# Kernel tuning notes

Measured on AMD Instinct MI355X. Metric: run time of the kernel, lower is better.

The kernel has to match this reference:

```python
import jax, jax.numpy as jnp
import numpy as np

B, D, E = 128, 1024, 1024   # batch, word_rnn_size, word_encoding_size
NV, NL = 36, 20             # visual regions, language memory slots
T = 4                       # max_att_step
EPS = 0.01                  # opt.epsilon
SCALE = 0.02


def _lstm_cell(x, h, c, Wih, Whh, bih, bhh):
    # torch.nn.LSTMCell gate order: i, f, g, o
    g = x @ Wih.T + bih + h @ Whh.T + bhh
    i, f, gg, o = jnp.split(g, 4, axis=-1)
    c2 = jax.nn.sigmoid(f) * c + jax.nn.sigmoid(i) * jnp.tanh(gg)
    h2 = jax.nn.sigmoid(o) * jnp.tanh(c2)
    return h2, c2


def _kv_attention(h_att, vkey, vval, lkey, lval, kvs):
    # stand-in for the externally-passed kv_attention module:
    # scaled dot-product attention over visual and language memories
    q = h_att + kvs                                   # [B,D]
    inv = 1.0 / np.sqrt(D)
    va = jax.nn.softmax(jnp.einsum('bnd,bd->bn', vkey, q) * inv, axis=-1)
    vctx = jnp.einsum('bn,bnd->bd', va, vval)
    la = jax.nn.softmax(jnp.einsum('bmd,bd->bm', lkey, q) * inv, axis=-1)
    lctx = jnp.einsum('bm,bmd->bd', la, lval)
    return vctx, lctx, jnp.tanh(kvs + vctx + lctx)


def _update_kv(out, vkey, lkey):
    # stand-in for the externally-passed update_kv module
    return vkey + 0.01 * out[:, None, :], lkey + 0.01 * out[:, None, :]


def _forward(xt, fc_feats, visual_value, visual_key, lang_value, lang_key,
             kv_state, state_h, state_c,
             att_Wih, att_Whh, att_bih, att_bhh,
             lang_Wih, lang_Whh, lang_bih, lang_bhh,
             conf_W1, conf_b1, conf_W2, conf_b2,
             it, max_att_step):
    word_exist = (it > 0).astype(jnp.float32)         # [B]
    prev_h = state_h[-1]
    # att_lstm input is constant across halting steps (state is not updated in the loop)
    att_in = jnp.concatenate([prev_h, fc_feats, xt], axis=1)  # [B, E+2D]
    z1 = jnp.zeros((B, 1), jnp.float32)
    zD = jnp.zeros((B, D), jnp.float32)
    zB = jnp.zeros((B,), jnp.float32)
    carry0 = (z1, jnp.ones((B, 1), jnp.float32), zD, zD, zD, zD, zD, zB,
              visual_key, lang_key, kv_state)

    def body(carry, i):
        accum, sel, hA, cA, hL, cL, outA, cost, vkey, lkey, kvs = carry
        h_att, c_att = _lstm_cell(att_in, state_h[0], state_c[0],
                                  att_Wih, att_Whh, att_bih, att_bhh)
        vctx, lctx, kvs = _kv_attention(h_att, vkey, visual_value, lkey, lang_value, kvs)
        lang_in = jnp.concatenate([vctx, lctx, h_att], axis=1)  # [B,3D]
        h_lang, c_lang = _lstm_cell(lang_in, state_h[1], state_c[1],
                                    lang_Wih, lang_Whh, lang_bih, lang_bhh)
        out = h_lang  # F.dropout in eval mode is identity
        vkey, lkey = _update_kv(out, vkey, lkey)
        # confidence MLP: Linear -> ReLU -> Linear -> Sigmoid
        p = jax.nn.sigmoid(jax.nn.relu(h_lang @ conf_W1.T + conf_b1) @ conf_W2.T + conf_b2)  # [B,1]
        beta = p * (1.0 - accum)
        accum = accum + beta * sel
        hA = hA + beta * h_att * sel
        cA = cA + beta * c_att * sel
        hL = hL + beta * h_lang * sel
        cL = cL + beta * c_lang * sel
        outA = outA + beta * out * sel
        cost = cost + (i + 1.0) * (1.0 - p[:, 0]) * sel[:, 0]
        sel = jax.lax.stop_gradient((accum < 1.0 - EPS).astype(jnp.float32)) * sel
        return (accum, sel, hA, cA, hL, cL, outA, cost, vkey, lkey, kvs), None

    carry, _ = jax.lax.scan(body, carry0, jnp.arange(max_att_step, dtype=jnp.float32))
    accum, sel, hA, cA, hL, cL, outA, cost, vkey, lkey, kvs = carry
    hA = hA / accum
    cA = cA / accum
    hL = hL / accum
    cL = cL / accum
    outA = outA / accum
    new_h = jnp.stack([hA, hL])
    new_c = jnp.stack([cA, cL])
    return outA, vkey, lkey, cost * word_exist, new_h, new_c, kvs


def setup_inputs() -> dict:
    ks = jax.random.split(jax.random.key(0), 20)
    n = lambda k, s, sc=1.0: jax.random.normal(k, s, dtype=jnp.float32) * sc
    return {
        'xt': n(ks[0], (B, E)),
        'it': jax.random.randint(ks[1], (B,), 0, 9487, dtype=jnp.int32),
        'fc_feats': n(ks[2], (B, D)),
        'visual_value': n(ks[3], (B, NV, D)),
        'visual_key': n(ks[4], (B, NV, D)),
        'lang_value': n(ks[5], (B, NL, D)),
        'lang_key': n(ks[6], (B, NL, D)),
        'kv_state': n(ks[7], (B, D)),
        'state_h': n(ks[8], (2, B, D)),
        'state_c': n(ks[9], (2, B, D)),
        'max_att_step': T,
        'att_Wih': n(ks[10], (4 * D, E + 2 * D), SCALE),
        'att_Whh': n(ks[11], (4 * D, D), SCALE),
        'att_bih': jnp.zeros((4 * D,), jnp.float32),
        'att_bhh': jnp.zeros((4 * D,), jnp.float32),
        'lang_Wih': n(ks[12], (4 * D, 3 * D), SCALE),
        'lang_Whh': n(ks[13], (4 * D, D), SCALE),
        'lang_bih': jnp.zeros((4 * D,), jnp.float32),
        'lang_bhh': jnp.zeros((4 * D,), jnp.float32),
        'conf_W1': n(ks[14], (D, D), SCALE),
        'conf_b1': jnp.zeros((D,), jnp.float32),
        'conf_W2': n(ks[15], (1, D), SCALE),
        'conf_b2': jnp.zeros((1,), jnp.float32),
    }


def reference(xt, it, fc_feats, visual_value, visual_key, lang_value, lang_key,
              kv_state, state_h, state_c, max_att_step,
              att_Wih, att_Whh, att_bih, att_bhh,
              lang_Wih, lang_Whh, lang_bih, lang_bhh,
              conf_W1, conf_b1, conf_W2, conf_b2):
    return _forward(xt, fc_feats, visual_value, visual_key, lang_value, lang_key,
                    kv_state, state_h, state_c,
                    att_Wih, att_Whh, att_bih, att_bhh,
                    lang_Wih, lang_Whh, lang_bih, lang_bhh,
                    conf_W1, conf_b1, conf_W2, conf_b2,
                    it, max_att_step)
```

## Files before the change

kernel.cpp:

```cpp
#include <hip/hip_runtime.h>
#include <hip/hip_bf16.h>

constexpr int B  = 128;
constexpr int D  = 1024;
constexpr int NV = 36;
constexpr int NL = 20;
constexpr int BD = B * D;
constexpr float EPS = 0.01f;
constexpr int NSLOT = 8;

constexpr long SL  = 524288;
constexpr long SLB = 2097152;
constexpr long OFF_GPA   = 0;
constexpr long OFF_GPLB  = OFF_GPA + 8 * SL;
constexpr long OFF_LBASE = OFF_GPLB + 8 * SL;
constexpr long OFF_GPB   = OFF_LBASE + SL;
constexpr long OFF_GPC0  = OFF_GPB + 2 * SLB;
constexpr long OFF_GPC1  = OFF_GPC0 + 524288;
constexpr long OFF_HATT2 = OFF_GPC1 + 524288;
constexpr long OFF_CATT2 = OFF_HATT2 + BD;
constexpr long OFF_HLB   = OFF_CATT2 + BD;
constexpr long OFF_CLB   = OFF_HLB + 524288;
constexpr long OFF_VCTXB = OFF_CLB + 524288;
constexpr long OFF_LCTXB = OFF_VCTXB + 524288;
constexpr long OFF_S2    = OFF_LCTXB + 524288;
constexpr long OFF_VVB   = OFF_S2 + BD;
constexpr long OFF_LVB   = OFF_VVB + 2359296;

typedef float f32x4 __attribute__((ext_vector_type(4)));
typedef short s16x8 __attribute__((ext_vector_type(8)));

__device__ __forceinline__ float sigf(float x) { return 1.f / (1.f + expf(-x)); }

__device__ __forceinline__ short f2bf(float f) {
  __hip_bfloat16 h = __float2bfloat16(f);
  return *reinterpret_cast<short*>(&h);
}
__device__ __forceinline__ float bf2f(short s) {
  unsigned u = ((unsigned)(unsigned short)s) << 16;
  return __uint_as_float(u);
}

__device__ __forceinline__ f32x4 LD4(const float* p) { return *(const f32x4*)p; }
__device__ __forceinline__ void ST4(float* p, f32x4 v) { *(f32x4*)p = v; }

struct GemmArgs {
  const float* A[NSLOT];
  const float* W[NSLOT];
  long wstride[NSLOT];
  int klen;
};

__global__ __launch_bounds__(256, 2) void gemm_mfma(GemmArgs ga, int N,
                                                    long pstride,
                                                    float* __restrict__ gpart) {
  const int z = blockIdx.z;
  const float* __restrict__ A = ga.A[z];
  const float* __restrict__ W = ga.W[z];
  const long wstr = ga.wstride[z];
  const int brow = blockIdx.y * 128;
  const int bcol = blockIdx.x * 64;
  float* __restrict__ out = gpart + (long)z * pstride;

  __shared__ __align__(16) short As[2][128][72];
  __shared__ __align__(16) short Bs[2][64][72];

  const int tid = threadIdx.x;
  const int wave = tid >> 6, lane = tid & 63;
  const int wr = wave >> 1, wc = wave & 1;
  const int lrow = lane & 15;
  const int lk8  = (lane >> 4) * 8;
  const int sr = tid >> 4;
  const int sc4 = (tid & 15) * 4;

  f32x4 acc[4][2];
#pragma unroll
  for (int m = 0; m < 4; ++m)
#pragma unroll
    for (int n = 0; n < 2; ++n) acc[m][n] = (f32x4){0.f, 0.f, 0.f, 0.f};

  float4 ra[8], rw[4];
#define LOAD_TILE(KT)                                                          \
  {                                                                            \
    const int kb = (KT) * 64;                                                  \
    _Pragma("unroll") for (int i = 0; i < 8; ++i) {                            \
      const int r = sr + i * 16;                                               \
      ra[i] = *(const float4*)(A + (long)(brow + r) * 1024 + kb + sc4);        \
    }                                                                          \
    _Pragma("unroll") for (int i = 0; i < 4; ++i) {                            \
      const int r = sr + i * 16;                                               \
      rw[i] = *(const float4*)(W + (long)(bcol + r) * wstr + kb + sc4);        \
    }                                                                          \
  }
#define WRITE_TILE(BUF)                                                        \
  {                                                                            \
    _Pragma("unroll") for (int i = 0; i < 8; ++i) {                            \
      const int r = sr + i * 16;                                               \
      *(short4*)(&As[BUF][r][sc4]) =                                           \
          short4{f2bf(ra[i].x), f2bf(ra[i].y), f2bf(ra[i].z), f2bf(ra[i].w)};  \
    }                                                                          \
    _Pragma("unroll") for (int i = 0; i < 4; ++i) {                            \
      const int r = sr + i * 16;                                               \
      *(short4*)(&Bs[BUF][r][sc4]) =                                           \
          short4{f2bf(rw[i].x), f2bf(rw[i].y), f2bf(rw[i].z), f2bf(rw[i].w)};  \
    }                                                                          \
  }

  const int ntiles = ga.klen / 64;
  LOAD_TILE(0);
  WRITE_TILE(0);
  __syncthreads();
  for (int kt = 0; kt < ntiles; ++kt) {
    const int cur = kt & 1;
    const bool more = (kt + 1 < ntiles);
    if (more) LOAD_TILE(kt + 1);
#pragma unroll
    for (int kk = 0; kk < 64; kk += 32) {
      s16x8 af[4], bf[2];
#pragma unroll
      for (int m = 0; m < 4; ++m)
        af[m] = *(const s16x8*)(&As[cur][wr * 64 + m * 16 + lrow][kk + lk8]);
#pragma unroll
      for (int n = 0; n < 2; ++n)
        bf[n] = *(const s16x8*)(&Bs[cur][wc * 32 + n * 16 + lrow][kk + lk8]);
#pragma unroll
      for (int m = 0; m < 4; ++m)
#pragma unroll
        for (int n = 0; n < 2; ++n)
          acc[m][n] = __builtin_amdgcn_mfma_f32_16x16x32_bf16(
              af[m], bf[n], acc[m][n], 0, 0, 0);
    }
    if (more) WRITE_TILE(1 - cur);
    __syncthreads();
  }
#undef LOAD_TILE
#undef WRITE_TILE

#pragma unroll
  for (int m = 0; m < 4; ++m) {
#pragma unroll
    for (int n = 0; n < 2; ++n) {
      const int col = bcol + wc * 32 + n * 16 + lrow;
#pragma unroll
      for (int r = 0; r < 4; ++r) {
        const int row = brow + wr * 64 + m * 16 + (lane >> 4) * 4 + r;
        out[(long)row * N + col] = acc[m][n][r];
      }
    }
  }
}

__global__ __launch_bounds__(256) void lstm_att(
    const float* __restrict__ gp, const float* __restrict__ bih,
    const float* __restrict__ bhh, const float* __restrict__ c_prev,
    float* __restrict__ h, float* __restrict__ c) {
  long idx = ((long)blockIdx.x * 256 + threadIdx.x) * 4;
  if (idx >= BD) return;
  int b = (int)(idx >> 10), d = (int)(idx & 1023);
  const long base = (long)b * 4096 + d;
  f32x4 g[4];
#pragma unroll
  for (int gi = 0; gi < 4; ++gi) {
    const long o = base + gi * 1024;
    f32x4 v = LD4(bih + gi * 1024 + d) + LD4(bhh + gi * 1024 + d);
#pragma unroll
    for (int s = 0; s < NSLOT; ++s) v += LD4(gp + s * SL + o);
    g[gi] = v;
  }
  f32x4 cp = LD4(c_prev + idx), cc, hh;
#pragma unroll
  for (int j = 0; j < 4; ++j) {
    float ccj = sigf(g[1][j]) * cp[j] + sigf(g[0][j]) * tanhf(g[2][j]);
    cc[j] = ccj;
    hh[j] = sigf(g[3][j]) * tanhf(ccj);
  }
  ST4(c + idx, cc);
  ST4(h + idx, hh);
}

__global__ __launch_bounds__(256) void reduce8(
    const float* __restrict__ gp, const float* __restrict__ bih,
    const float* __restrict__ bhh, float* __restrict__ out) {
  long idx = ((long)blockIdx.x * 256 + threadIdx.x) * 4;
  if (idx >= (long)B * 4096) return;
  int col = (int)(idx & 4095);
  f32x4 v = LD4(bih + col) + LD4(bhh + col);
#pragma unroll
  for (int s = 0; s < NSLOT; ++s) v += LD4(gp + s * SL + idx);
  ST4(out + idx, v);
}

__global__ __launch_bounds__(1024) void attn_mega(
    const float* __restrict__ h_att, const float* __restrict__ kv0,
    const float* __restrict__ vkey, const float* __restrict__ lkey,
    const float* __restrict__ vval, const float* __restrict__ lval,
    float* __restrict__ vctxB, float* __restrict__ lctxB,
    __hip_bfloat16* __restrict__ vvb, __hip_bfloat16* __restrict__ lvb,
    float* __restrict__ out_kvs) {
  const int b = blockIdx.x, tid = threadIdx.x;
  __shared__ short K[56][1024];
  __shared__ float q[1024];
  __shared__ float wgt[64];
  const int wave = tid >> 6, lane = tid & 63;

  for (int i = tid; i < 56 * 256; i += 1024) {
    const int r = i >> 8, c4 = (i & 255) * 4;
    const float* kp = (r < NV) ? vkey + ((long)b * NV + r) * 1024
                               : lkey + ((long)b * NL + (r - NV)) * 1024;
    float4 v = *(const float4*)(kp + c4);
    *(short4*)(&K[r][c4]) = short4{f2bf(v.x), f2bf(v.y), f2bf(v.z), f2bf(v.w)};
  }

  const float ha = h_att[(long)b * 1024 + tid];
  float kv = kv0[(long)b * 1024 + tid];

  for (int step = 0; step < 4; ++step) {
    q[tid] = ha + kv;
    __syncthreads();
    for (int n = wave; n < NV + NL; n += 16) {
      float s = 0.f;
#pragma unroll
      for (int j = 0; j < 2; ++j) {
        const int base = lane * 8 + j * 512;
        s16x8 k8 = *(const s16x8*)(&K[n][base]);
        f32x4 q0 = *(const f32x4*)(&q[base]);
        f32x4 q1 = *(const f32x4*)(&q[base + 4]);
#pragma unroll
        for (int e = 0; e < 4; ++e) {
          s += bf2f(k8[e]) * q0[e];
          s += bf2f(k8[e + 4]) * q1[e];
        }
      }
      for (int m = 32; m >= 1; m >>= 1) s += __shfl_xor(s, m);
      if (lane == 0) wgt[n] = s * (1.0f / 32.0f);
    }
    __syncthreads();
    if (wave == 0) {
      float x = (lane < NV) ? wgt[lane] : -1e30f;
      float m = x;
      for (int k = 32; k >= 1; k >>= 1) m = fmaxf(m, __shfl_xor(m, k));
      float e = (lane < NV) ? expf(x - m) : 0.f;
      float ssum = e;
      for (int k = 32; k >= 1; k >>= 1) ssum += __shfl_xor(ssum, k);
      if (lane < NV) wgt[lane] = e / ssum;
    } else if (wave == 1) {
      float x = (lane < NL) ? wgt[NV + lane] : -1e30f;
      float m = x;
      for (int k = 32; k >= 1; k >>= 1) m = fmaxf(m, __shfl_xor(m, k));
      float e = (lane < NL) ? expf(x - m) : 0.f;
      float ssum = e;
      for (int k = 32; k >= 1; k >>= 1) ssum += __shfl_xor(ssum, k);
      if (lane < NL) wgt[NV + lane] = e / ssum;
    }
    __syncthreads();
    float vc = 0.f, lc = 0.f;
    if (step == 0) {
      const float* vp = vval + (long)b * NV * 1024 + tid;
      __hip_bfloat16* vb = vvb + (long)b * NV * 1024 + tid;
#pragma unroll 6
      for (int n = 0; n < NV; ++n) {
        float v = vp[(long)n * 1024];
        vc += v * wgt[n];
        vb[(long)n * 1024] = __float2bfloat16(v);
      }
      const float* lp = lval + (long)b * NL * 1024 + tid;
      __hip_bfloat16* lb = lvb + (long)b * NL * 1024 + tid;
#pragma unroll 5
      for (int n = 0; n < NL; ++n) {
        float v = lp[(long)n * 1024];
        lc += v * wgt[NV + n];
        lb[(long)n * 1024] = __float2bfloat16(v);
      }
    } else {
      const __hip_bfloat16* vb = vvb + (long)b * NV * 1024 + tid;
#pragma unroll 6
      for (int n = 0; n < NV; ++n)
        vc += __bfloat162float(vb[(long)n * 1024]) * wgt[n];
      const __hip_bfloat16* lb = lvb + (long)b * NL * 1024 + tid;
#pragma unroll 5
      for (int n = 0; n < NL; ++n)
        lc += __bfloat162float(lb[(long)n * 1024]) * wgt[NV + n];
    }
    const long orow = ((long)step * 128 + b) * 1024 + tid;
    vctxB[orow] = vc;
    lctxB[orow] = lc;
    kv = tanhf(kv + vc + lc);
    __syncthreads();
  }
  out_kvs[(long)b * 1024 + tid] = kv;
}

__global__ __launch_bounds__(256) void lstm_batch(
    const float* __restrict__ gpB, const float* __restrict__ lbase,
    const float* __restrict__ sc1, float* __restrict__ hB,
    float* __restrict__ cB) {
  long idx = ((long)blockIdx.x * 256 + threadIdx.x) * 4;
  if (idx >= 512L * 1024) return;
  const int row = (int)(idx >> 10);
  const int b = row & 127;
  const int d = (int)(idx & 1023);
  const long base = (long)row * 4096 + d;
  const long lbbase = (long)b * 4096 + d;
  f32x4 g[4];
#pragma unroll
  for (int gi = 0; gi < 4; ++gi) {
    const long o = gi * 1024;
    g[gi] = LD4(gpB + base + o) + LD4(gpB + SLB + base + o) +
            LD4(lbase + lbbase + o);
  }
  f32x4 cp = LD4(sc1 + (long)b * 1024 + d), cc, hh;
#pragma unroll
  for (int j = 0; j < 4; ++j) {
    float ccj = sigf(g[1][j]) * cp[j] + sigf(g[0][j]) * tanhf(g[2][j]);
    cc[j] = ccj;
    hh[j] = sigf(g[3][j]) * tanhf(ccj);
  }
  ST4(cB + idx, cc);
  ST4(hB + idx, hh);
}

constexpr long O1 = BD;
constexpr long O2 = O1 + (long)B * NV * D;
constexpr long O3 = O2 + (long)B * NL * D;
constexpr long O4 = O3 + B;
constexpr long O5 = O4 + 2L * BD;
constexpr long O6 = O5 + 2L * BD;
constexpr long O7 = O6 + BD;

__global__ __launch_bounds__(256) void halt_scan(
    const float* __restrict__ gpc0, const float* __restrict__ gpc1,
    const float* __restrict__ cb1, const float* __restrict__ W2,
    const float* __restrict__ b2, const float* __restrict__ hB,
    const float* __restrict__ cB, const int* __restrict__ it,
    float* __restrict__ Sout, float* __restrict__ out) {
  const int b = blockIdx.x, tid = threadIdx.x;
  const int d0 = tid * 4;
  __shared__ float red[256];
  __shared__ float p_sh;
  const f32x4 w4 = LD4(W2 + d0);
  const f32x4 cb = LD4(cb1 + d0);
  f32x4 hl_acc = (f32x4){0.f, 0.f, 0.f, 0.f}, cl_acc = hl_acc, s_acc = hl_acc;
  float a = 0.f, sel = 1.f, cost = 0.f;

  for (int i = 0; i < 4; ++i) {
    const long o = ((long)i * 128 + b) * 1024 + d0;
    f32x4 rv = LD4(gpc0 + o) + LD4(gpc1 + o) + cb;
    float part = 0.f;
#pragma unroll
    for (int j = 0; j < 4; ++j) part += fmaxf(rv[j], 0.f) * w4[j];
    red[tid] = part;
    __syncthreads();
    for (int s = 128; s > 0; s >>= 1) {
      if (tid < s) red[tid] += red[tid + s];
      __syncthreads();
    }
    if (tid == 0) p_sh = sigf(red[0] + b2[0]);
    __syncthreads();
    const float p = p_sh;
    const float bs = p * (1.f - a) * sel;
    f32x4 hl = LD4(hB + o), cl = LD4(cB + o);
    hl_acc += hl * bs;
    cl_acc += cl * bs;
    s_acc += hl;
    cost += (float)(i + 1) * (1.f - p) * sel;
    a += bs;
    sel = (a < 1.f - EPS) ? sel : 0.f;
    __syncthreads();
  }
  const float inv_a = 1.f / a;
  const long ob = (long)b * 1024 + d0;
  ST4(out + ob, hl_acc * inv_a);
  ST4(out + O4 + BD + ob, hl_acc * inv_a);
  ST4(out + O5 + BD + ob, cl_acc * inv_a);
  ST4(Sout + ob, s_acc);
  if (tid == 0) out[O3 + b] = cost * ((it[b] > 0) ? 1.f : 0.f);
}

constexpr long VK = (long)B * NV * D;
constexpr long LK = (long)B * NL * D;

__global__ __launch_bounds__(256) void finalize2(
    const float* __restrict__ vkey0, const float* __restrict__ lkey0,
    const float* __restrict__ S, const float* __restrict__ h_att,
    const float* __restrict__ c_att, float* __restrict__ out) {
  long idx = ((long)blockIdx.x * 256 + threadIdx.x) * 4;
  if (idx < VK) {
    int b = (int)(idx / (NV * 1024));
    int d = (int)(idx & 1023);
    ST4(out + O1 + idx, LD4(vkey0 + idx) + LD4(S + (long)b * 1024 + d) * 0.01f);
  } else if (idx < VK + LK) {
    long r = idx - VK;
    int b = (int)(r / (NL * 1024));
    int d = (int)(r & 1023);
    ST4(out + O2 + r, LD4(lkey0 + r) + LD4(S + (long)b * 1024 + d) * 0.01f);
  } else if (idx < VK + LK + BD) {
    long r = idx - VK - LK;
    ST4(out + O4 + r, LD4(h_att + r));
  } else if (idx < VK + LK + 2L * BD) {
    long r = idx - VK - LK - BD;
    ST4(out + O5 + r, LD4(c_att + r));
  }
}

extern "C" void kernel_launch(void* const* d_in, const int* in_sizes, int n_in,
                              void* d_out, int out_size, void* d_ws, size_t ws_size,
                              hipStream_t stream) {
  const float* xt   = (const float*)d_in[0];
  const int*   it   = (const int*)d_in[1];
  const float* fc   = (const float*)d_in[2];
  const float* vval = (const float*)d_in[3];
  const float* vkey = (const float*)d_in[4];
  const float* lval = (const float*)d_in[5];
  const float* lkey = (const float*)d_in[6];
  const float* kv0  = (const float*)d_in[7];
  const float* sh   = (const float*)d_in[8];
  const float* sc   = (const float*)d_in[9];
  const float* aWih = (const float*)d_in[11];
  const float* aWhh = (const float*)d_in[12];
  const float* abih = (const float*)d_in[13];
  const float* abhh = (const float*)d_in[14];
  const float* lWih = (const float*)d_in[15];
  const float* lWhh = (const float*)d_in[16];
  const float* lbih = (const float*)d_in[17];
  const float* lbhh = (const float*)d_in[18];
  const float* cW1  = (const float*)d_in[19];
  const float* cb1  = (const float*)d_in[20];
  const float* cW2  = (const float*)d_in[21];
  const float* cb2  = (const float*)d_in[22];

  float* ws = (float*)d_ws;
  float* gpA   = ws + OFF_GPA;
  float* gpLB  = ws + OFF_GPLB;
  float* lbase = ws + OFF_LBASE;
  float* gpB   = ws + OFF_GPB;
  float* gpC0  = ws + OFF_GPC0;
  float* gpC1  = ws + OFF_GPC1;
  float* h_att = ws + OFF_HATT2;
  float* c_att = ws + OFF_CATT2;
  float* hB    = ws + OFF_HLB;
  float* cB    = ws + OFF_CLB;
  float* vctxB = ws + OFF_VCTXB;
  float* lctxB = ws + OFF_LCTXB;
  float* Sbuf  = ws + OFF_S2;
  __hip_bfloat16* vvb = (__hip_bfloat16*)(ws + OFF_VVB);
  __hip_bfloat16* lvb = (__hip_bfloat16*)(ws + OFF_LVB);

  const float* sh1 = sh + BD;
  const float* sc0 = sc;
  const float* sc1 = sc + BD;
  float* out = (float*)d_out;

  {
    GemmArgs ga;
    ga.A[0] = sh1;       ga.W[0] = aWih;        ga.wstride[0] = 3072;
    ga.A[1] = sh1 + 512; ga.W[1] = aWih + 512;  ga.wstride[1] = 3072;
    ga.A[2] = fc;        ga.W[2] = aWih + 1024; ga.wstride[2] = 3072;
    ga.A[3] = fc + 512;  ga.W[3] = aWih + 1536; ga.wstride[3] = 3072;
    ga.A[4] = xt;        ga.W[4] = aWih + 2048; ga.wstride[4] = 3072;
    ga.A[5] = xt + 512;  ga.W[5] = aWih + 2560; ga.wstride[5] = 3072;
    ga.A[6] = sh;        ga.W[6] = aWhh;        ga.wstride[6] = 1024;
    ga.A[7] = sh + 512;  ga.W[7] = aWhh + 512;  ga.wstride[7] = 1024;
    ga.klen = 512;
    gemm_mfma<<<dim3(64, 1, 8), 256, 0, stream>>>(ga, 4096, SL, gpA);
  }
  lstm_att<<<128, 256, 0, stream>>>(gpA, abih, abhh, sc0, h_att, c_att);

  {
    GemmArgs ga;
#pragma unroll
    for (int q = 0; q < 4; ++q) {
      ga.A[q] = sh1 + q * 256;
      ga.W[q] = lWhh + q * 256;
      ga.wstride[q] = 1024;
      ga.A[4 + q] = h_att + q * 256;
      ga.W[4 + q] = lWih + 2048 + q * 256;
      ga.wstride[4 + q] = 3072;
    }
    ga.klen = 256;
    gemm_mfma<<<dim3(64, 1, 8), 256, 0, stream>>>(ga, 4096, SL, gpLB);
  }
  reduce8<<<512, 256, 0, stream>>>(gpLB, lbih, lbhh, lbase);

  attn_mega<<<128, 1024, 0, stream>>>(h_att, kv0, vkey, lkey, vval, lval,
                                      vctxB, lctxB, vvb, lvb, out + O6);

  {
    GemmArgs ga;
    ga.A[0] = vctxB; ga.W[0] = lWih;        ga.wstride[0] = 3072;
    ga.A[1] = lctxB; ga.W[1] = lWih + 1024; ga.wstride[1] = 3072;
#pragma unroll
    for (int z = 2; z < 8; ++z) { ga.A[z] = vctxB; ga.W[z] = lWih; ga.wstride[z] = 3072; }
    ga.klen = 1024;
    gemm_mfma<<<dim3(64, 4, 2), 256, 0, stream>>>(ga, 4096, SLB, gpB);
  }
  lstm_batch<<<512, 256, 0, stream>>>(gpB, lbase, sc1, hB, cB);

  {
    GemmArgs ga;
    ga.A[0] = hB;       ga.W[0] = cW1;       ga.wstride[0] = 1024;
    ga.A[1] = hB + 512; ga.W[1] = cW1 + 512; ga.wstride[1] = 1024;
#pragma unroll
    for (int z = 2; z < 8; ++z) { ga.A[z] = hB; ga.W[z] = cW1; ga.wstride[z] = 1024; }
    ga.klen = 512;
    gemm_mfma<<<dim3(16, 4, 2), 256, 0, stream>>>(ga, 1024, 524288, gpC0);
  }
  halt_scan<<<128, 256, 0, stream>>>(gpC0, gpC1, cb1, cW2, cb2, hB, cB, it,
                                     Sbuf, out);
  finalize2<<<7424, 256, 0, stream>>>(vkey, lkey, Sbuf, h_att, c_att, out);
}
```

Baseline: 148.0 us.

## Overlap bf16 conversion of attention memories with first gate GEMM

Adds extra blocks to the first gate GEMM launch that convert the visual and language keys and values to bf16 in workspace. These blocks run concurrently with the GEMM, so the fp32 conversion no longer happens inside the 128-block attention kernel. The attention kernel now loads pre-converted bf16 keys and values and uses four-way split accumulators. The LSTM-att kernel writes h_att and c_att straight to the output, which removes that copy from the finalize kernel. The trade-off is extra workspace and extra memory traffic for a full bf16 copy of the keys.

```diff
diff --git a/kernel.cpp b/kernel.cpp
--- a/kernel.cpp
+++ b/kernel.cpp
@@ -26,6 +26,8 @@
 constexpr long OFF_S2    = OFF_LCTXB + 524288;
 constexpr long OFF_VVB   = OFF_S2 + BD;
 constexpr long OFF_LVB   = OFF_VVB + 2359296;
+constexpr long OFF_VKB   = OFF_LVB + 1310720;
+constexpr long OFF_LKB   = OFF_VKB + 2359296;
 
 typedef float f32x4 __attribute__((ext_vector_type(4)));
 typedef short s16x8 __attribute__((ext_vector_type(8)));
@@ -51,9 +53,11 @@
   int klen;
 };
 
-__global__ __launch_bounds__(256, 2) void gemm_mfma(GemmArgs ga, int N,
-                                                    long pstride,
-                                                    float* __restrict__ gpart) {
+__device__ __forceinline__ void gemm_body(const GemmArgs& ga, int N,
+                                          long pstride,
+                                          float* __restrict__ gpart) {
+  __shared__ __align__(16) short As[2][128][72];
+  __shared__ __align__(16) short Bs[2][64][72];
   const int z = blockIdx.z;
   const float* __restrict__ A = ga.A[z];
   const float* __restrict__ W = ga.W[z];
@@ -61,9 +65,6 @@
   const int brow = blockIdx.y * 128;
   const int bcol = blockIdx.x * 64;
   float* __restrict__ out = gpart + (long)z * pstride;
-
-  __shared__ __align__(16) short As[2][128][72];
-  __shared__ __align__(16) short Bs[2][64][72];
 
   const int tid = threadIdx.x;
   const int wave = tid >> 6, lane = tid & 63;
@@ -150,10 +151,53 @@
   }
 }
 
+__global__ __launch_bounds__(256, 2) void gemm_mfma(GemmArgs ga, int N,
+                                                    long pstride,
+                                                    float* __restrict__ gpart) {
+  gemm_body(ga, N, pstride, gpart);
+}
+
+__device__ __forceinline__ void conv_bf16(const float* __restrict__ src,
+                                          __hip_bfloat16* __restrict__ dst,
+                                          long nelem, int bid, int nb) {
+  const long total = nelem >> 2;
+  for (long i = (long)bid * 256 + threadIdx.x; i < total; i += (long)nb * 256) {
+    f32x4 v = LD4(src + i * 4);
+    *(short4*)((short*)dst + i * 4) =
+        short4{f2bf(v[0]), f2bf(v[1]), f2bf(v[2]), f2bf(v[3])};
+  }
+}
+
+__global__ __launch_bounds__(256, 2) void gemmA_prestage(
+    GemmArgs ga, int N, long pstride, float* __restrict__ gpart,
+    const float* __restrict__ vkey, const float* __restrict__ lkey,
+    const float* __restrict__ vval, const float* __restrict__ lval,
+    __hip_bfloat16* __restrict__ vkb, __hip_bfloat16* __restrict__ lkb,
+    __hip_bfloat16* __restrict__ vvb, __hip_bfloat16* __restrict__ lvb) {
+  if (blockIdx.z < 8) {
+    gemm_body(ga, N, pstride, gpart);
+  } else {
+    const int bid = (blockIdx.z - 8) * 64 + blockIdx.x;
+    const int nb = 256;
+    conv_bf16(vkey, vkb, (long)B * NV * 1024, bid, nb);
+    conv_bf16(lkey, lkb, (long)B * NL * 1024, bid, nb);
+    conv_bf16(vval, vvb, (long)B * NV * 1024, bid, nb);
+    conv_bf16(lval, lvb, (long)B * NL * 1024, bid, nb);
+  }
+}
+
+constexpr long O1 = BD;
+constexpr long O2 = O1 + (long)B * NV * D;
+constexpr long O3 = O2 + (long)B * NL * D;
+constexpr long O4 = O3 + B;
+constexpr long O5 = O4 + 2L * BD;
+constexpr long O6 = O5 + 2L * BD;
+constexpr long O7 = O6 + BD;
+
 __global__ __launch_bounds__(256) void lstm_att(
     const float* __restrict__ gp, const float* __restrict__ bih,
     const float* __restrict__ bhh, const float* __restrict__ c_prev,
-    float* __restrict__ h, float* __restrict__ c) {
+    float* __restrict__ h, float* __restrict__ c, float* __restrict__ out) {
   long idx = ((long)blockIdx.x * 256 + threadIdx.x) * 4;
   if (idx >= BD) return;
   int b = (int)(idx >> 10), d = (int)(idx & 1023);
@@ -176,6 +220,8 @@
   }
   ST4(c + idx, cc);
   ST4(h + idx, hh);
+  ST4(out + O4 + idx, hh);
+  ST4(out + O5 + idx, cc);
 }
 
 __global__ __launch_bounds__(256) void reduce8(
@@ -192,10 +238,9 @@
 
 __global__ __launch_bounds__(1024) void attn_mega(
     const float* __restrict__ h_att, const float* __restrict__ kv0,
-    const float* __restrict__ vkey, const float* __restrict__ lkey,
-    const float* __restrict__ vval, const float* __restrict__ lval,
+    const __hip_bfloat16* __restrict__ vkb, const __hip_bfloat16* __restrict__ lkb,
+    const __hip_bfloat16* __restrict__ vvb, const __hip_bfloat16* __restrict__ lvb,
     float* __restrict__ vctxB, float* __restrict__ lctxB,
-    __hip_bfloat16* __restrict__ vvb, __hip_bfloat16* __restrict__ lvb,
     float* __restrict__ out_kvs) {
   const int b = blockIdx.x, tid = threadIdx.x;
   __shared__ short K[56][1024];
@@ -203,12 +248,12 @@
   __shared__ float wgt[64];
   const int wave = tid >> 6, lane = tid & 63;
 
-  for (int i = tid; i < 56 * 256; i += 1024) {
-    const int r = i >> 8, c4 = (i & 255) * 4;
-    const float* kp = (r < NV) ? vkey + ((long)b * NV + r) * 1024
-                               : lkey + ((long)b * NL + (r - NV)) * 1024;
-    float4 v = *(const float4*)(kp + c4);
-    *(short4*)(&K[r][c4]) = short4{f2bf(v.x), f2bf(v.y), f2bf(v.z), f2bf(v.w)};
+  for (int i = tid; i < 56 * 128; i += 1024) {
+    const int r = i >> 7, c8 = (i & 127) * 8;
+    const __hip_bfloat16* kp = (r < NV)
+        ? vkb + ((long)b * NV + r) * 1024
+        : lkb + ((long)b * NL + (r - NV)) * 1024;
+    *(s16x8*)(&K[r][c8]) = *(const s16x8*)(kp + c8);
   }
 
   const float ha = h_att[(long)b * 1024 + tid];
@@ -253,34 +298,26 @@
       if (lane < NL) wgt[NV + lane] = e / ssum;
     }
     __syncthreads();
-    float vc = 0.f, lc = 0.f;
-    if (step == 0) {
-      const float* vp = vval + (long)b * NV * 1024 + tid;
-      __hip_bfloat16* vb = vvb + (long)b * NV * 1024 + tid;
-#pragma unroll 6
-      for (int n = 0; n < NV; ++n) {
-        float v = vp[(long)n * 1024];
-        vc += v * wgt[n];
-        vb[(long)n * 1024] = __float2bfloat16(v);
-      }
-      const float* lp = lval + (long)b * NL * 1024 + tid;
-      __hip_bfloat16* lb = lvb + (long)b * NL * 1024 + tid;
-#pragma unroll 5
-      for (int n = 0; n < NL; ++n) {
-        float v = lp[(long)n * 1024];
-        lc += v * wgt[NV + n];
-        lb[(long)n * 1024] = __float2bfloat16(v);
-      }
-    } else {
-      const __hip_bfloat16* vb = vvb + (long)b * NV * 1024 + tid;
-#pragma unroll 6
-      for (int n = 0; n < NV; ++n)
-        vc += __bfloat162float(vb[(long)n * 1024]) * wgt[n];
-      const __hip_bfloat16* lb = lvb + (long)b * NL * 1024 + tid;
-#pragma unroll 5
-      for (int n = 0; n < NL; ++n)
-        lc += __bfloat162float(lb[(long)n * 1024]) * wgt[NV + n];
-    }
+    const __hip_bfloat16* vb = vvb + (long)b * NV * 1024 + tid;
+    float a0 = 0.f, a1 = 0.f, a2 = 0.f, a3 = 0.f;
+#pragma unroll
+    for (int n = 0; n < NV; n += 4) {
+      a0 += __bfloat162float(vb[(long)(n + 0) * 1024]) * wgt[n + 0];
+      a1 += __bfloat162float(vb[(long)(n + 1) * 1024]) * wgt[n + 1];
+      a2 += __bfloat162float(vb[(long)(n + 2) * 1024]) * wgt[n + 2];
+      a3 += __bfloat162float(vb[(long)(n + 3) * 1024]) * wgt[n + 3];
+    }
+    const float vc = (a0 + a1) + (a2 + a3);
+    const __hip_bfloat16* lb = lvb + (long)b * NL * 1024 + tid;
+    float c0 = 0.f, c1 = 0.f, c2 = 0.f, c3 = 0.f;
+#pragma unroll
+    for (int n = 0; n < NL; n += 4) {
+      c0 += __bfloat162float(lb[(long)(n + 0) * 1024]) * wgt[NV + n + 0];
+      c1 += __bfloat162float(lb[(long)(n + 1) * 1024]) * wgt[NV + n + 1];
+      c2 += __bfloat162float(lb[(long)(n + 2) * 1024]) * wgt[NV + n + 2];
+      c3 += __bfloat162float(lb[(long)(n + 3) * 1024]) * wgt[NV + n + 3];
+    }
+    const float lc = (c0 + c1) + (c2 + c3);
     const long orow = ((long)step * 128 + b) * 1024 + tid;
     vctxB[orow] = vc;
     lctxB[orow] = lc;
@@ -318,14 +355,6 @@
   ST4(cB + idx, cc);
   ST4(hB + idx, hh);
 }
-
-constexpr long O1 = BD;
-constexpr long O2 = O1 + (long)B * NV * D;
-constexpr long O3 = O2 + (long)B * NL * D;
-constexpr long O4 = O3 + B;
-constexpr long O5 = O4 + 2L * BD;
-constexpr long O6 = O5 + 2L * BD;
-constexpr long O7 = O6 + BD;
 
 __global__ __launch_bounds__(256) void halt_scan(
     const float* __restrict__ gpc0, const float* __restrict__ gpc1,
@@ -381,8 +410,7 @@
 
 __global__ __launch_bounds__(256) void finalize2(
     const float* __restrict__ vkey0, const float* __restrict__ lkey0,
-    const float* __restrict__ S, const float* __restrict__ h_att,
-    const float* __restrict__ c_att, float* __restrict__ out) {
+    const float* __restrict__ S, float* __restrict__ out) {
   long idx = ((long)blockIdx.x * 256 + threadIdx.x) * 4;
   if (idx < VK) {
     int b = (int)(idx / (NV * 1024));
@@ -393,12 +421,6 @@
     int b = (int)(r / (NL * 1024));
     int d = (int)(r & 1023);
     ST4(out + O2 + r, LD4(lkey0 + r) + LD4(S + (long)b * 1024 + d) * 0.01f);
-  } else if (idx < VK + LK + BD) {
-    long r = idx - VK - LK;
-    ST4(out + O4 + r, LD4(h_att + r));
-  } else if (idx < VK + LK + 2L * BD) {
-    long r = idx - VK - LK - BD;
-    ST4(out + O5 + r, LD4(c_att + r));
   }
 }
 
@@ -444,6 +466,8 @@
   float* Sbuf  = ws + OFF_S2;
   __hip_bfloat16* vvb = (__hip_bfloat16*)(ws + OFF_VVB);
   __hip_bfloat16* lvb = (__hip_bfloat16*)(ws + OFF_LVB);
+  __hip_bfloat16* vkb = (__hip_bfloat16*)(ws + OFF_VKB);
+  __hip_bfloat16* lkb = (__hip_bfloat16*)(ws + OFF_LKB);
 
   const float* sh1 = sh + BD;
   const float* sc0 = sc;
@@ -461,9 +485,10 @@
     ga.A[6] = sh;        ga.W[6] = aWhh;        ga.wstride[6] = 1024;
     ga.A[7] = sh + 512;  ga.W[7] = aWhh + 512;  ga.wstride[7] = 1024;
     ga.klen = 512;
-    gemm_mfma<<<dim3(64, 1, 8), 256, 0, stream>>>(ga, 4096, SL, gpA);
-  }
-  lstm_att<<<128, 256, 0, stream>>>(gpA, abih, abhh, sc0, h_att, c_att);
+    gemmA_prestage<<<dim3(64, 1, 12), 256, 0, stream>>>(
+        ga, 4096, SL, gpA, vkey, lkey, vval, lval, vkb, lkb, vvb, lvb);
+  }
+  lstm_att<<<128, 256, 0, stream>>>(gpA, abih, abhh, sc0, h_att, c_att, out);
 
   {
     GemmArgs ga;
@@ -481,8 +506,8 @@
   }
   reduce8<<<512, 256, 0, stream>>>(gpLB, lbih, lbhh, lbase);
 
-  attn_mega<<<128, 1024, 0, stream>>>(h_att, kv0, vkey, lkey, vval, lval,
-                                      vctxB, lctxB, vvb, lvb, out + O6);
+  attn_mega<<<128, 1024, 0, stream>>>(h_att, kv0, vkb, lkb, vvb, lvb,
+                                      vctxB, lctxB, out + O6);
 
   {
     GemmArgs ga;
@@ -506,5 +531,5 @@
   }
   halt_scan<<<128, 256, 0, stream>>>(gpC0, gpC1, cb1, cW2, cb2, hB, cB, it,
                                      Sbuf, out);
-  finalize2<<<7424, 256, 0, stream>>>(vkey, lkey, Sbuf, h_att, c_att, out);
-}
+  finalize2<<<7168, 256, 0, stream>>>(vkey, lkey, Sbuf, out);
+}
```

New measurement: 160.6 us. 8.5% more time.
